# Kernel optimization log

Measured on AMD Instinct MI355X. Metric: run time of the kernel, lower is better.

The kernel has to match this reference:

```python
import jax, jax.numpy as jnp
import numpy as np

S, L, D = 128, 512, 256   # MSA rows, residues, msa_dim
H, C = 8, 32              # num_heads, head_dim


def setup_inputs() -> dict:
    key = jax.random.key(0)
    ks = jax.random.split(key, 8)
    inp = {
        "msa_input": jax.random.normal(ks[0], (S, L, D), dtype=jnp.float32),
        "ln_scale": jnp.ones((D,), jnp.float32),
        "ln_bias": jnp.zeros((D,), jnp.float32),
        "wq": jax.random.normal(ks[1], (D, H * C), jnp.float32) / np.sqrt(D),
        "wk": jax.random.normal(ks[2], (D, H * C), jnp.float32) / np.sqrt(D),
        "wv": jax.random.normal(ks[3], (D, H * C), jnp.float32) / np.sqrt(D),
        "wg": jax.random.normal(ks[4], (D, H * C), jnp.float32) / np.sqrt(D),
        "bg": jnp.zeros((H * C,), jnp.float32),
        "wo": jax.random.normal(ks[5], (H * C, D), jnp.float32) / np.sqrt(H * C),
        "bo": jnp.zeros((D,), jnp.float32),
    }
    return inp


def reference(msa_input, ln_scale, ln_bias, wq, wk, wv, wg, bg, wo, bo):
    # LayerNorm over last dim (eps matches torch default 1e-5)
    mu = jnp.mean(msa_input, axis=-1, keepdims=True)
    var = jnp.mean(jnp.square(msa_input - mu), axis=-1, keepdims=True)
    x = (msa_input - mu) * jax.lax.rsqrt(var + 1e-5) * ln_scale + ln_bias

    q = (x @ wq).reshape(S, L, H, C)
    k = (x @ wk).reshape(S, L, H, C)
    v = (x @ wv).reshape(S, L, H, C)
    g = jax.nn.sigmoid(x @ wg + bg).reshape(S, L, H, C)

    scale = 1.0 / np.sqrt(C)
    # attention over MSA-row axis, per residue l and head h
    scores = jnp.einsum("slhc,tlhc->stlh", q, k) * scale   # [S,S,L,H]
    probs = jax.nn.softmax(scores, axis=1)                  # softmax over t
    o = jnp.einsum("stlh,tlhc->slhc", probs, v) * g         # [S,L,H,C]
    return o.reshape(S, L, H * C) @ wo + bo
```

## Files before the change

### kernel.cpp

```cpp
#include <hip/hip_runtime.h>
#include <hip/hip_bf16.h>

typedef __bf16 bf16;
typedef __bf16 bf16x8 __attribute__((ext_vector_type(8)));
typedef float f32x4 __attribute__((ext_vector_type(4)));

#define S_DIM 128
#define L_DIM 512
#define D_DIM 256
#define NQ    1024

__device__ __forceinline__ void gl16(void* lds, const void* g) {
  __builtin_amdgcn_global_load_lds((const __attribute__((address_space(1))) void*)g,
                                   (__attribute__((address_space(3))) void*)lds,
                                   16, 0, 0);
}

__global__ void pack_weights(const float* __restrict__ wq, const float* __restrict__ wk,
                             const float* __restrict__ wv, const float* __restrict__ wg,
                             const float* __restrict__ wo,
                             bf16* __restrict__ wcat_t, bf16* __restrict__ wo_t) {
  int idx = blockIdx.x * 256 + threadIdx.x;
  const int total1 = NQ * D_DIM;
  if (idx < total1) {
    int j = idx >> 8;
    int d = idx & 255;
    const float* w = (j < 256) ? wq : (j < 512) ? wk : (j < 768) ? wv : wg;
    wcat_t[idx] = (bf16)w[d * 256 + (j & 255)];
  } else {
    int i2 = idx - total1;
    if (i2 < D_DIM * D_DIM) {
      int dcol = i2 >> 8, k = i2 & 255;
      wo_t[i2] = (bf16)wo[k * 256 + dcol];
    }
  }
}

__global__ __launch_bounds__(512, 4) void ln_qkvg(const float* __restrict__ msa,
                                                  const float* __restrict__ lns,
                                                  const float* __restrict__ lnb,
                                                  const bf16* __restrict__ wcat,
                                                  const float* __restrict__ bg,
                                                  bf16* __restrict__ pan) {
  __shared__ __align__(16) char smem[81920];
  bf16* Albs = (bf16*)smem;
  char* Bb   = smem;
  bf16* Cst  = (bf16*)(smem + 65536);
  const int tid  = threadIdx.x;
  const int wid  = tid >> 6;
  const int lane = tid & 63;
  const int lrow = lane & 15;
  const int lkg  = lane >> 4;
  const int lk   = lkg * 8;
  const int rb   = lkg * 4;
  const int res  = blockIdx.x;

  {
    float4 scv = ((const float4*)lns)[lane];
    float4 bsv = ((const float4*)lnb)[lane];
    const float* mbase = msa + ((size_t)(wid * 16) * 512 + res) * 256 + lane * 4;
    #pragma unroll
    for (int b4 = 0; b4 < 4; ++b4) {
      float4 rv[4];
      #pragma unroll
      for (int i = 0; i < 4; ++i)
        rv[i] = *(const float4*)(mbase + (size_t)(b4 * 4 + i) * 512 * 256);
      #pragma unroll
      for (int i = 0; i < 4; ++i) {
        int s = wid * 16 + b4 * 4 + i;
        float4 v = rv[i];
        float sum = v.x + v.y + v.z + v.w;
        #pragma unroll
        for (int m = 32; m; m >>= 1) sum += __shfl_xor(sum, m);
        float mu = sum * (1.0f / 256.0f);
        float dx = v.x - mu, dy = v.y - mu, dz = v.z - mu, dw = v.w - mu;
        float s2 = dx * dx + dy * dy + dz * dz + dw * dw;
        #pragma unroll
        for (int m = 32; m; m >>= 1) s2 += __shfl_xor(s2, m);
        float rs = rsqrtf(s2 * (1.0f / 256.0f) + 1e-5f);
        union { uint2 u; bf16 b[4]; } o;
        o.b[0] = (bf16)(dx * rs * scv.x + bsv.x);
        o.b[1] = (bf16)(dy * rs * scv.y + bsv.y);
        o.b[2] = (bf16)(dz * rs * scv.z + bsv.z);
        o.b[3] = (bf16)(dw * rs * scv.w + bsv.w);
        *(uint2*)((char*)Albs + (((s * 512) + lane * 8) ^ ((s & 7) << 4))) = o.u;
      }
    }
  }
  __syncthreads();

  const int mq = wid & 3;
  const int nh = wid >> 2;
  bf16x8 afc[2][8];
  #pragma unroll
  for (int mt = 0; mt < 2; ++mt)
    #pragma unroll
    for (int kk = 0; kk < 8; ++kk) {
      int row = mq * 32 + mt * 16 + lrow;
      afc[mt][kk] = *(const bf16x8*)((char*)Albs +
                      (((row * 512) + (kk * 32 + lk) * 2) ^ ((row & 7) << 4)));
    }
  __syncthreads();

  #pragma unroll
  for (int p = 0; p < 4; ++p) {
    int ch = p * 512 + tid;
    int n = ch >> 5;
    int inner = (ch & 31) * 16;
    gl16(Bb + p * 8192 + wid * 1024,
         (const char*)wcat + (size_t)n * 512 + (inner ^ ((n & 7) << 4)));
  }
  __syncthreads();

  for (int cc = 0; cc < 16; ++cc) {
    char* Bcur = Bb + (cc & 1) * 32768;
    f32x4 acc[2][2] = {};
    #pragma unroll
    for (int kk = 0; kk < 8; ++kk) {
      bf16x8 bv[2];
      #pragma unroll
      for (int nt = 0; nt < 2; ++nt) {
        int nl = nh * 32 + nt * 16 + lrow;
        bv[nt] = *(const bf16x8*)(Bcur +
                    (((nl * 512) + (kk * 32 + lk) * 2) ^ ((nl & 7) << 4)));
      }
      #pragma unroll
      for (int mt = 0; mt < 2; ++mt)
        #pragma unroll
        for (int nt = 0; nt < 2; ++nt)
          acc[mt][nt] = __builtin_amdgcn_mfma_f32_16x16x32_bf16(afc[mt][kk], bv[nt], acc[mt][nt], 0, 0, 0);
    }
    if (cc < 15) {
      char* Bnxt = Bb + ((cc + 1) & 1) * 32768;
      const size_t ncol0 = (size_t)(cc + 1) * 64;
      #pragma unroll
      for (int p = 0; p < 4; ++p) {
        int ch = p * 512 + tid;
        int n = ch >> 5;
        int inner = (ch & 31) * 16;
        gl16(Bnxt + p * 8192 + wid * 1024,
             (const char*)wcat + (ncol0 + n) * 512 + (inner ^ ((n & 7) << 4)));
      }
    }
    const bool isg = (cc >= 12);
    #pragma unroll
    for (int mt = 0; mt < 2; ++mt)
      #pragma unroll
      for (int nt = 0; nt < 2; ++nt) {
        int col = nh * 32 + nt * 16 + lrow;
        float bgv = isg ? bg[(cc - 12) * 64 + col] : 0.f;
        #pragma unroll
        for (int r = 0; r < 4; ++r) {
          int row = mq * 32 + mt * 16 + rb + r;
          float v = acc[mt][nt][r];
          if (isg) { v += bgv; v = 1.0f / (1.0f + __expf(-v)); }
          Cst[row * 64 + (col ^ (rb << 2))] = (bf16)v;
        }
      }
    __syncthreads();
    {
      const int type = cc >> 2, hp = cc & 3;
      bf16* pbase = pan + ((size_t)((type * 512 + res) * 4) + hp) * 8192;
      #pragma unroll
      for (int p = 0; p < 2; ++p) {
        int ch = p * 512 + tid;
        int rr = ch >> 3, c16 = ch & 7;
        *(uint4*)(pbase + rr * 64 + c16 * 8) =
            *(const uint4*)(Cst + rr * 64 + ((c16 * 8) ^ ((rr & 12) << 2)));
      }
    }
    asm volatile("s_waitcnt lgkmcnt(0)" ::: "memory");
    __builtin_amdgcn_s_barrier();
  }
}

__global__ __launch_bounds__(512, 2) void attn_proj(const bf16* __restrict__ pan,
                                                    const bf16* __restrict__ wo_t,
                                                    const float* __restrict__ bo,
                                                    float* __restrict__ out) {
  __shared__ __align__(16) char smem[155648];
  const int tid  = threadIdx.x;
  const int wid  = tid >> 6;
  const int lane = tid & 63;
  const int lrow = lane & 15;
  const int lkg  = lane >> 4;
  const int lk   = lkg * 8;
  const int rb   = lkg * 4;
  const int res  = blockIdx.x;
  const int h    = wid;
  const int hp   = h >> 1;
  const int hl   = (h & 1) * 32;

  bf16* vw  = (bf16*)(smem + wid * 8704);
  bf16* pwb = (bf16*)(smem + 69632 + wid * 2304);
  bf16* of  = (bf16*)(smem + 88064);

  const bf16* Pq = pan + ((size_t)((0 * 512 + res) * 4) + hp) * 8192 + hl;
  const bf16* Pk = pan + ((size_t)((1 * 512 + res) * 4) + hp) * 8192 + hl;
  const bf16* Pv = pan + ((size_t)((2 * 512 + res) * 4) + hp) * 8192 + hl;

  {
    int t0 = lane >> 2, cs = (lane & 3) * 8;
    #pragma unroll
    for (int p = 0; p < 8; ++p) {
      int t = p * 16 + t0;
      union { uint4 u; bf16 e[8]; } v;
      v.u = *(const uint4*)(Pv + t * 64 + cs);
      #pragma unroll
      for (int j = 0; j < 8; ++j) vw[(cs + j) * 136 + t] = v.e[j];
    }
  }

  bf16x8 kf[8];
  #pragma unroll
  for (int tt = 0; tt < 8; ++tt)
    kf[tt] = *(const bf16x8*)(Pk + (tt * 16 + lrow) * 64 + lk);

  const float scale = 0.17677669529663687f;
  const f32x4 z = {0.f, 0.f, 0.f, 0.f};

  for (int st = 0; st < 8; ++st) {
    bf16x8 qf = *(const bf16x8*)(Pq + (st * 16 + lrow) * 64 + lk);
    f32x4 sc[8];
    #pragma unroll
    for (int tt = 0; tt < 8; ++tt)
      sc[tt] = __builtin_amdgcn_mfma_f32_16x16x32_bf16(qf, kf[tt], z, 0, 0, 0);

    #pragma unroll
    for (int r = 0; r < 4; ++r) {
      float m = sc[0][r];
      #pragma unroll
      for (int tc = 1; tc < 8; ++tc) m = fmaxf(m, sc[tc][r]);
      #pragma unroll
      for (int msk = 8; msk; msk >>= 1) m = fmaxf(m, __shfl_xor(m, msk));
      float pv[8], ssum = 0.f;
      #pragma unroll
      for (int tc = 0; tc < 8; ++tc) {
        float p = __expf((sc[tc][r] - m) * scale);
        pv[tc] = p; ssum += p;
      }
      #pragma unroll
      for (int msk = 8; msk; msk >>= 1) ssum += __shfl_xor(ssum, msk);
      float inv = 1.0f / ssum;
      #pragma unroll
      for (int tc = 0; tc < 8; ++tc) sc[tc][r] = pv[tc] * inv;
    }

    f32x4 oc[2] = {z, z};
    #pragma unroll
    for (int hf = 0; hf < 2; ++hf) {
      #pragma unroll
      for (int tc = 0; tc < 4; ++tc)
        #pragma unroll
        for (int r = 0; r < 4; ++r)
          pwb[(rb + r) * 72 + tc * 16 + lrow] = (bf16)sc[hf * 4 + tc][r];
      #pragma unroll
      for (int kc = 0; kc < 2; ++kc) {
        bf16x8 pa = *(const bf16x8*)(pwb + lrow * 72 + kc * 32 + lk);
        #pragma unroll
        for (int ct = 0; ct < 2; ++ct) {
          bf16x8 bv = *(const bf16x8*)(vw + (ct * 16 + lrow) * 136 + hf * 64 + kc * 32 + lk);
          oc[ct] = __builtin_amdgcn_mfma_f32_16x16x32_bf16(pa, bv, oc[ct], 0, 0, 0);
        }
      }
    }
    #pragma unroll
    for (int ct = 0; ct < 2; ++ct)
      #pragma unroll
      for (int r = 0; r < 4; ++r)
        of[(st * 16 + rb + r) * 264 + h * 32 + ct * 16 + lrow] = (bf16)oc[ct][r];
  }
  __syncthreads();

  const int wm = wid >> 1;
  const int pn = wid & 1;

  bf16x8 af[2][8];
  #pragma unroll
  for (int mt = 0; mt < 2; ++mt) {
    int s = wm * 32 + mt * 16 + lrow;
    #pragma unroll
    for (int kt = 0; kt < 8; ++kt) {
      bf16x8 o8 = *(const bf16x8*)(of + s * 264 + kt * 32 + lk);
      bf16x8 g8 = *(const bf16x8*)(pan + ((size_t)((3 * 512 + res) * 4) + (kt >> 1)) * 8192 +
                                   (kt & 1) * 32 + s * 64 + lk);
      bf16x8 rr;
      #pragma unroll
      for (int j = 0; j < 8; ++j) rr[j] = (bf16)((float)o8[j] * (float)g8[j]);
      af[mt][kt] = rr;
    }
  }

  float bov[2][4];
  #pragma unroll
  for (int hf = 0; hf < 2; ++hf)
    #pragma unroll
    for (int nt = 0; nt < 4; ++nt)
      bov[hf][nt] = bo[hf * 128 + pn * 64 + nt * 16 + lrow];

  bf16* wS = (bf16*)smem;
  f32x4 acc[2][2][4] = {};
  #pragma unroll
  for (int hf = 0; hf < 2; ++hf) {
    #pragma unroll
    for (int p = 0; p < 8; ++p) {
      int ch = p * 512 + tid;
      int dl = ch >> 5, sl = ch & 31;
      gl16((char*)wS + p * 8192 + wid * 1024,
           (const char*)wo_t + (size_t)(hf * 128 + dl) * 512 + (((sl * 16) ^ ((dl & 7) << 4))));
    }
    __syncthreads();
    #pragma unroll
    for (int kt = 0; kt < 8; ++kt)
      #pragma unroll
      for (int nt = 0; nt < 4; ++nt) {
        int dl = pn * 64 + nt * 16 + lrow;
        bf16x8 bw = *(const bf16x8*)((char*)wS + dl * 512 + (((kt * 4 + lkg) ^ (dl & 7)) << 4));
        acc[hf][0][nt] = __builtin_amdgcn_mfma_f32_16x16x32_bf16(af[0][kt], bw, acc[hf][0][nt], 0, 0, 0);
        acc[hf][1][nt] = __builtin_amdgcn_mfma_f32_16x16x32_bf16(af[1][kt], bw, acc[hf][1][nt], 0, 0, 0);
      }
    __syncthreads();
  }

  float* fb = (float*)smem;
  #pragma unroll 1
  for (int b = 0; b < 4; ++b) {
    if (wm == b) {
      #pragma unroll
      for (int hf = 0; hf < 2; ++hf)
        #pragma unroll
        for (int mt = 0; mt < 2; ++mt)
          #pragma unroll
          for (int nt = 0; nt < 4; ++nt)
            #pragma unroll
            for (int r = 0; r < 4; ++r)
              fb[(mt * 16 + rb + r) * 264 + hf * 128 + pn * 64 + nt * 16 + lrow] =
                  acc[hf][mt][nt][r] + bov[hf][nt];
    }
    __syncthreads();
    #pragma unroll
    for (int u = 0; u < 4; ++u) {
      int ch = u * 512 + tid;
      int row = ch >> 6, c4 = (ch & 63) * 4;
      *(uint4*)(out + ((size_t)(b * 32 + row) * L_DIM + res) * 256 + c4) =
          *(const uint4*)(fb + row * 264 + c4);
    }
    __syncthreads();
  }
}

extern "C" void kernel_launch(void* const* d_in, const int* in_sizes, int n_in,
                              void* d_out, int out_size, void* d_ws, size_t ws_size,
                              hipStream_t stream) {
  const float* msa      = (const float*)d_in[0];
  const float* ln_scale = (const float*)d_in[1];
  const float* ln_bias  = (const float*)d_in[2];
  const float* wq       = (const float*)d_in[3];
  const float* wk       = (const float*)d_in[4];
  const float* wv       = (const float*)d_in[5];
  const float* wg       = (const float*)d_in[6];
  const float* bg       = (const float*)d_in[7];
  const float* wo       = (const float*)d_in[8];
  const float* bo       = (const float*)d_in[9];
  float* out = (float*)d_out;

  char* ws = (char*)d_ws;
  bf16* wcat_t = (bf16*)ws;
  bf16* wo_t   = (bf16*)(ws + 524288);
  bf16* pan    = (bf16*)(ws + 655360);

  pack_weights<<<dim3(1280), dim3(256), 0, stream>>>(wq, wk, wv, wg, wo, wcat_t, wo_t);
  ln_qkvg<<<dim3(512), dim3(512), 0, stream>>>(msa, ln_scale, ln_bias, wcat_t, bg, pan);
  attn_proj<<<dim3(512), dim3(512), 0, stream>>>(pan, wo_t, bo, out);
}
```

Before: 138.8 us.

## Split fused attention+projection kernel into separate attention and GEMM kernels

Replaces the fused per-residue attention-plus-output-projection kernel (512 threads, about 152KB of LDS) with two kernels. The first is a 256-thread attention kernel over half the heads, using XOR-swizzled LDS; it applies the gate and writes a bf16 intermediate to a new global workspace buffer. The second is a standalone 128x128-tiled GEMM that does the output projection and bias add. The aim is higher occupancy and less LDS pressure, at the cost of an extra global round trip for the intermediate, a second launch, and a larger workspace requirement.

Result: no change. 140.9 us (+1.5%).

```diff
diff --git a/kernel.cpp b/kernel.cpp
--- a/kernel.cpp
+++ b/kernel.cpp
@@ -174,11 +174,9 @@
   }
 }
 
-__global__ __launch_bounds__(512, 2) void attn_proj(const bf16* __restrict__ pan,
-                                                    const bf16* __restrict__ wo_t,
-                                                    const float* __restrict__ bo,
-                                                    float* __restrict__ out) {
-  __shared__ __align__(16) char smem[155648];
+__global__ __launch_bounds__(256, 4) void attn_kernel(const bf16* __restrict__ pan,
+                                                      bf16* __restrict__ obuf) {
+  __shared__ __align__(16) char smem[40960];
   const int tid  = threadIdx.x;
   const int wid  = tid >> 6;
   const int lane = tid & 63;
@@ -186,18 +184,21 @@
   const int lkg  = lane >> 4;
   const int lk   = lkg * 8;
   const int rb   = lkg * 4;
-  const int res  = blockIdx.x;
-  const int h    = wid;
+  const int bid  = blockIdx.x;
+  const int rest = bid >> 3;
+  const int hg   = rest & 1;
+  const int res  = (bid & 7) | ((rest >> 1) << 3);
+  const int h    = hg * 4 + wid;
   const int hp   = h >> 1;
   const int hl   = (h & 1) * 32;
 
-  bf16* vw  = (bf16*)(smem + wid * 8704);
-  bf16* pwb = (bf16*)(smem + 69632 + wid * 2304);
-  bf16* of  = (bf16*)(smem + 88064);
+  char* vw  = smem + wid * 8192;
+  char* pwb = smem + 32768 + wid * 2048;
 
   const bf16* Pq = pan + ((size_t)((0 * 512 + res) * 4) + hp) * 8192 + hl;
   const bf16* Pk = pan + ((size_t)((1 * 512 + res) * 4) + hp) * 8192 + hl;
   const bf16* Pv = pan + ((size_t)((2 * 512 + res) * 4) + hp) * 8192 + hl;
+  const bf16* Pg = pan + ((size_t)((3 * 512 + res) * 4) + hp) * 8192 + hl;
 
   {
     int t0 = lane >> 2, cs = (lane & 3) * 8;
@@ -207,7 +208,10 @@
       union { uint4 u; bf16 e[8]; } v;
       v.u = *(const uint4*)(Pv + t * 64 + cs);
       #pragma unroll
-      for (int j = 0; j < 8; ++j) vw[(cs + j) * 136 + t] = v.e[j];
+      for (int j = 0; j < 8; ++j) {
+        int c = cs + j;
+        *(bf16*)(vw + ((c * 256 + t * 2) ^ ((c & 7) << 4))) = v.e[j];
+      }
     }
   }
 
@@ -252,100 +256,129 @@
       #pragma unroll
       for (int tc = 0; tc < 4; ++tc)
         #pragma unroll
-        for (int r = 0; r < 4; ++r)
-          pwb[(rb + r) * 72 + tc * 16 + lrow] = (bf16)sc[hf * 4 + tc][r];
+        for (int r = 0; r < 4; ++r) {
+          int row = rb + r, col = tc * 16 + lrow;
+          *(bf16*)(pwb + ((row * 128 + col * 2) ^ ((row & 7) << 4))) = (bf16)sc[hf * 4 + tc][r];
+        }
       #pragma unroll
       for (int kc = 0; kc < 2; ++kc) {
-        bf16x8 pa = *(const bf16x8*)(pwb + lrow * 72 + kc * 32 + lk);
+        bf16x8 pa = *(const bf16x8*)(pwb + ((lrow * 128 + (kc * 32 + lk) * 2) ^ ((lrow & 7) << 4)));
         #pragma unroll
         for (int ct = 0; ct < 2; ++ct) {
-          bf16x8 bv = *(const bf16x8*)(vw + (ct * 16 + lrow) * 136 + hf * 64 + kc * 32 + lk);
+          int c = ct * 16 + lrow;
+          bf16x8 bv = *(const bf16x8*)(vw + ((c * 256 + (hf * 64 + kc * 32 + lk) * 2) ^ ((c & 7) << 4)));
           oc[ct] = __builtin_amdgcn_mfma_f32_16x16x32_bf16(pa, bv, oc[ct], 0, 0, 0);
         }
       }
     }
+
     #pragma unroll
     for (int ct = 0; ct < 2; ++ct)
       #pragma unroll
-      for (int r = 0; r < 4; ++r)
-        of[(st * 16 + rb + r) * 264 + h * 32 + ct * 16 + lrow] = (bf16)oc[ct][r];
-  }
-  __syncthreads();
-
-  const int wm = wid >> 1;
-  const int pn = wid & 1;
-
-  bf16x8 af[2][8];
-  #pragma unroll
-  for (int mt = 0; mt < 2; ++mt) {
-    int s = wm * 32 + mt * 16 + lrow;
-    #pragma unroll
-    for (int kt = 0; kt < 8; ++kt) {
-      bf16x8 o8 = *(const bf16x8*)(of + s * 264 + kt * 32 + lk);
-      bf16x8 g8 = *(const bf16x8*)(pan + ((size_t)((3 * 512 + res) * 4) + (kt >> 1)) * 8192 +
-                                   (kt & 1) * 32 + s * 64 + lk);
-      bf16x8 rr;
-      #pragma unroll
-      for (int j = 0; j < 8; ++j) rr[j] = (bf16)((float)o8[j] * (float)g8[j]);
-      af[mt][kt] = rr;
-    }
-  }
-
-  float bov[2][4];
-  #pragma unroll
-  for (int hf = 0; hf < 2; ++hf)
-    #pragma unroll
-    for (int nt = 0; nt < 4; ++nt)
-      bov[hf][nt] = bo[hf * 128 + pn * 64 + nt * 16 + lrow];
-
-  bf16* wS = (bf16*)smem;
-  f32x4 acc[2][2][4] = {};
-  #pragma unroll
-  for (int hf = 0; hf < 2; ++hf) {
+      for (int r = 0; r < 4; ++r) {
+        int row = rb + r, c = ct * 16 + lrow;
+        *(bf16*)(pwb + ((row * 128 + c * 2) ^ ((row & 7) << 4))) = (bf16)oc[ct][r];
+      }
+    {
+      int row = lane >> 2, cb = lane & 3;
+      union { uint4 u; bf16 e[8]; } o8, g8, r8;
+      o8.u = *(const uint4*)(pwb + ((row * 128 + cb * 16) ^ ((row & 7) << 4)));
+      g8.u = *(const uint4*)(Pg + (st * 16 + row) * 64 + cb * 8);
+      #pragma unroll
+      for (int u = 0; u < 8; ++u) r8.e[u] = (bf16)((float)o8.e[u] * (float)g8.e[u]);
+      *(uint4*)(obuf + ((size_t)res * 128 + st * 16 + row) * 256 + h * 32 + cb * 8) = r8.u;
+    }
+  }
+}
+
+__global__ __launch_bounds__(256, 4) void gemm_proj(const bf16* __restrict__ A,
+                                                    const bf16* __restrict__ Bt,
+                                                    float* __restrict__ Cout,
+                                                    const float* __restrict__ bias) {
+  __shared__ __align__(16) bf16 smem[16384];
+  bf16* As = smem;
+  bf16* Bs = smem + 8192;
+  const int tid  = threadIdx.x;
+  const int wid  = tid >> 6;
+  const int lane = tid & 63;
+  const int bid   = blockIdx.x;
+  const int n_idx = (bid >> 3) & 1;
+  const int m_idx = (bid & 7) | ((bid >> 4) << 3);
+  const int m0 = m_idx * 128;
+  const int n0 = n_idx * 128;
+  const int lrow = lane & 15;
+  const int lk   = (lane >> 4) * 8;
+  const int wr = wid >> 1, wc = wid & 1;
+
+  const int ln8 = lane >> 3;
+  const int c8  = ((lane & 7) ^ ln8) * 8;
+
+  const bf16* Arow = A  + (size_t)m0 * 256 + c8;
+  const bf16* Brow = Bt + (size_t)n0 * 256 + c8;
+
+  f32x4 acc[4][4] = {};
+
+  #pragma unroll
+  for (int ks = 0; ks < 4; ++ks) {
+    const int k0 = ks * 64;
+    #pragma unroll
+    for (int t = 0; t < 4; ++t) {
+      int chunk = wid * 4 + t;
+      int r = chunk * 8 + ln8;
+      gl16(&As[chunk * 512], Arow + (size_t)r * 256 + k0);
+      gl16(&Bs[chunk * 512], Brow + (size_t)r * 256 + k0);
+    }
+    __syncthreads();
+    #pragma unroll
+    for (int kk = 0; kk < 64; kk += 32) {
+      bf16x8 av[4], bv[4];
+      #pragma unroll
+      for (int i = 0; i < 4; ++i)
+        av[i] = *(const bf16x8*)((const char*)As + ((((wr * 64 + i * 16 + lrow) * 128) + (kk + lk) * 2) ^ (((wr * 64 + i * 16 + lrow) & 7) << 4)));
+      #pragma unroll
+      for (int j = 0; j < 4; ++j)
+        bv[j] = *(const bf16x8*)((const char*)Bs + ((((wc * 64 + j * 16 + lrow) * 128) + (kk + lk) * 2) ^ (((wc * 64 + j * 16 + lrow) & 7) << 4)));
+      #pragma unroll
+      for (int i = 0; i < 4; ++i)
+        #pragma unroll
+        for (int j = 0; j < 4; ++j)
+          acc[i][j] = __builtin_amdgcn_mfma_f32_16x16x32_bf16(av[i], bv[j], acc[i][j], 0, 0, 0);
+    }
+    __syncthreads();
+  }
+
+  const int rb = (lane >> 4) * 4;
+  const int xorv = rb << 2;
+  float* smf = (float*)smem;
+  float bov[4];
+  #pragma unroll
+  for (int j = 0; j < 4; ++j) bov[j] = bias[n0 + wc * 64 + j * 16 + lrow];
+  #pragma unroll
+  for (int half = 0; half < 2; ++half) {
+    if (half) __syncthreads();
+    #pragma unroll
+    for (int i2 = 0; i2 < 2; ++i2) {
+      int i = half * 2 + i2;
+      #pragma unroll
+      for (int j = 0; j < 4; ++j) {
+        int col = wc * 64 + j * 16 + lrow;
+        #pragma unroll
+        for (int r = 0; r < 4; ++r) {
+          int crow = wr * 32 + i2 * 16 + rb + r;
+          smf[crow * 128 + (col ^ xorv)] = acc[i][j][r] + bov[j];
+        }
+      }
+    }
+    __syncthreads();
     #pragma unroll
     for (int p = 0; p < 8; ++p) {
-      int ch = p * 512 + tid;
-      int dl = ch >> 5, sl = ch & 31;
-      gl16((char*)wS + p * 8192 + wid * 1024,
-           (const char*)wo_t + (size_t)(hf * 128 + dl) * 512 + (((sl * 16) ^ ((dl & 7) << 4))));
-    }
-    __syncthreads();
-    #pragma unroll
-    for (int kt = 0; kt < 8; ++kt)
-      #pragma unroll
-      for (int nt = 0; nt < 4; ++nt) {
-        int dl = pn * 64 + nt * 16 + lrow;
-        bf16x8 bw = *(const bf16x8*)((char*)wS + dl * 512 + (((kt * 4 + lkg) ^ (dl & 7)) << 4));
-        acc[hf][0][nt] = __builtin_amdgcn_mfma_f32_16x16x32_bf16(af[0][kt], bw, acc[hf][0][nt], 0, 0, 0);
-        acc[hf][1][nt] = __builtin_amdgcn_mfma_f32_16x16x32_bf16(af[1][kt], bw, acc[hf][1][nt], 0, 0, 0);
-      }
-    __syncthreads();
-  }
-
-  float* fb = (float*)smem;
-  #pragma unroll 1
-  for (int b = 0; b < 4; ++b) {
-    if (wm == b) {
-      #pragma unroll
-      for (int hf = 0; hf < 2; ++hf)
-        #pragma unroll
-        for (int mt = 0; mt < 2; ++mt)
-          #pragma unroll
-          for (int nt = 0; nt < 4; ++nt)
-            #pragma unroll
-            for (int r = 0; r < 4; ++r)
-              fb[(mt * 16 + rb + r) * 264 + hf * 128 + pn * 64 + nt * 16 + lrow] =
-                  acc[hf][mt][nt][r] + bov[hf][nt];
-    }
-    __syncthreads();
-    #pragma unroll
-    for (int u = 0; u < 4; ++u) {
-      int ch = u * 512 + tid;
-      int row = ch >> 6, c4 = (ch & 63) * 4;
-      *(uint4*)(out + ((size_t)(b * 32 + row) * L_DIM + res) * 256 + c4) =
-          *(const uint4*)(fb + row * 264 + c4);
-    }
-    __syncthreads();
+      int ch = p * 256 + tid;
+      int crow = ch >> 5, slot = (ch & 31) * 4;
+      int rx = (crow & 12) << 2;
+      int s_loc = (crow >> 5) * 64 + half * 32 + (crow & 31);
+      *(uint4*)(Cout + ((size_t)s_loc * 512 + m_idx) * 256 + n0 + slot) =
+          *(const uint4*)(smf + crow * 128 + (slot ^ rx));
+    }
   }
 }
 
@@ -368,8 +401,10 @@
   bf16* wcat_t = (bf16*)ws;
   bf16* wo_t   = (bf16*)(ws + 524288);
   bf16* pan    = (bf16*)(ws + 655360);
+  bf16* obuf   = (bf16*)(ws + 655360 + 134217728ULL);
 
   pack_weights<<<dim3(1280), dim3(256), 0, stream>>>(wq, wk, wv, wg, wo, wcat_t, wo_t);
   ln_qkvg<<<dim3(512), dim3(512), 0, stream>>>(msa, ln_scale, ln_bias, wcat_t, bg, pan);
-  attn_proj<<<dim3(512), dim3(512), 0, stream>>>(pan, wo_t, bo, out);
-}
+  attn_kernel<<<dim3(1024), dim3(256), 0, stream>>>(pan, obuf);
+  gemm_proj<<<dim3(1024), dim3(256), 0, stream>>>(obuf, wo_t, out, bo);
+}
```
